# Performance work log

Measured on AMD Instinct MI355X. Metric: run time of the kernel, lower is better.

The kernel has to match this reference:

```python
import jax, jax.numpy as jnp
import numpy as np

NTYPES = 8
EXCLUDE = [(0, 1), (2, 3)]
NF, NLOC, NNEI = 4, 16384, 128
NALL = 32768


def _build_type_mask(ntypes, exclude):
    ex = set()
    for a, b in exclude:
        ex.add((a, b))
        ex.add((b, a))
    tm = np.ones((ntypes + 1, ntypes + 1), dtype=np.float32)
    for ti, tj in ex:
        tm[tj, ti] = 0.0
    return tm.reshape(-1)  # flattened [(ntypes+1)^2]


def setup_inputs() -> dict:
    key = jax.random.key(0)
    k1, k2 = jax.random.split(key)
    # nlist in [-1, NALL): -1 marks a missing neighbor
    nlist = jax.random.randint(k1, (NF, NLOC, NNEI), -1, NALL, dtype=jnp.int32)
    atype_ext = jax.random.randint(k2, (NF, NALL), 0, NTYPES, dtype=jnp.int32)
    type_mask = jnp.asarray(_build_type_mask(NTYPES, EXCLUDE))
    return {"nlist": nlist, "atype_ext": atype_ext, "type_mask": type_mask, "ntypes": NTYPES}


def reference(nlist, atype_ext, type_mask, ntypes):
    nf, nloc, nnei = nlist.shape
    nall = atype_ext.shape[1]
    # append virtual type `ntypes` used for -1 (padding) neighbors
    ae = jnp.concatenate(
        [atype_ext, jnp.full((nf, 1), ntypes, dtype=atype_ext.dtype)], axis=-1
    )  # [nf, nall+1]
    type_i = atype_ext[:, :nloc] * (ntypes + 1)  # [nf, nloc]
    index = jnp.where(nlist == -1, nall, nlist)  # [nf, nloc, nnei]
    type_j = jnp.take_along_axis(ae, index.reshape(nf, nloc * nnei), axis=1)
    type_j = type_j.reshape(nf, nloc, nnei)
    type_ij = type_i[:, :, None] + type_j  # flat index into type_mask table
    mask = type_mask[type_ij]  # [nf, nloc, nnei]
    return mask
```

## Files before the change

kernel.cpp:

```cpp
#include <hip/hip_runtime.h>

#define NF    4
#define NLOC  16384
#define NNEI  128
#define NALL  32768
#define TMASK_LDS 96

#define ELEMS_PER_FRAME (NLOC * NNEI)
#define Q4_PER_FRAME    (ELEMS_PER_FRAME / 4)
#define BLOCKS_PER_FRAME 256
#define THREADS 256
#define ITERS (Q4_PER_FRAME / (BLOCKS_PER_FRAME * THREADS))

__global__ void __launch_bounds__(256) build_type_table(
    const int* __restrict__ atype_ext,
    unsigned char* __restrict__ ttab)
{
    const int t = blockIdx.x * blockDim.x + threadIdx.x;
    const int4 v = reinterpret_cast<const int4*>(atype_ext)[t];
    uchar4 b;
    b.x = (unsigned char)v.x;
    b.y = (unsigned char)v.y;
    b.z = (unsigned char)v.z;
    b.w = (unsigned char)v.w;
    reinterpret_cast<uchar4*>(ttab)[t] = b;
}

__global__ void __launch_bounds__(THREADS) pair_exclude_mask_kernel(
    const int* __restrict__ nlist,
    const unsigned char* __restrict__ ttab,
    const float* __restrict__ type_mask,
    const int* __restrict__ ntypes_p,
    float* __restrict__ out)
{
    __shared__ unsigned char stt[NALL];
    __shared__ float smask[TMASK_LDS];

    const int f = blockIdx.x / BLOCKS_PER_FRAME;
    const int b = blockIdx.x % BLOCKS_PER_FRAME;

    {
        const uint4* src = reinterpret_cast<const uint4*>(ttab + (size_t)f * NALL);
        uint4* dst = reinterpret_cast<uint4*>(stt);
        #pragma unroll
        for (int k = 0; k < NALL / 16 / THREADS; ++k)
            dst[threadIdx.x + k * THREADS] = src[threadIdx.x + k * THREADS];
        if (threadIdx.x < 81) smask[threadIdx.x] = type_mask[threadIdx.x];
    }
    __syncthreads();

    const int ntypes = ntypes_p[0];
    const int np1 = ntypes + 1;

    const int* nl_base = nlist + (size_t)f * ELEMS_PER_FRAME;
    float* out_base = out + (size_t)f * ELEMS_PER_FRAME;
    const int q0 = b * (THREADS * ITERS);

    #pragma unroll
    for (int it = 0; it < ITERS; ++it) {
        const int q = q0 + it * THREADS + threadIdx.x;
        const int4 nl = reinterpret_cast<const int4*>(nl_base)[q];
        const int e = q * 4;
        const int i = e >> 7;
        const int ti = (int)stt[i] * np1;

        float4 m;
        {
            const int tj = (nl.x == -1) ? ntypes : (int)stt[nl.x];
            m.x = smask[ti + tj];
        }
        {
            const int tj = (nl.y == -1) ? ntypes : (int)stt[nl.y];
            m.y = smask[ti + tj];
        }
        {
            const int tj = (nl.z == -1) ? ntypes : (int)stt[nl.z];
            m.z = smask[ti + tj];
        }
        {
            const int tj = (nl.w == -1) ? ntypes : (int)stt[nl.w];
            m.w = smask[ti + tj];
        }
        reinterpret_cast<float4*>(out_base)[q] = m;
    }
}

extern "C" void kernel_launch(void* const* d_in, const int* in_sizes, int n_in,
                              void* d_out, int out_size, void* d_ws, size_t ws_size,
                              hipStream_t stream) {
    const int*   nlist     = (const int*)d_in[0];
    const int*   atype_ext = (const int*)d_in[1];
    const float* type_mask = (const float*)d_in[2];
    const int*   ntypes_p  = (const int*)d_in[3];
    float*       out       = (float*)d_out;
    unsigned char* ttab    = (unsigned char*)d_ws;

    build_type_table<<<(NF * NALL / 4) / 256, 256, 0, stream>>>(atype_ext, ttab);

    pair_exclude_mask_kernel<<<NF * BLOCKS_PER_FRAME, THREADS, 0, stream>>>(
        nlist, ttab, type_mask, ntypes_p, out);
}
```

Measured before the change: 91.21 us.

## Precompute per-atom column bitmasks so mask lookup becomes a bit test

The preprocessing kernel now stores, for each extended atom, a byte bitmask over center types showing which pairs are allowed, plus a padding entry for the virtual -1 neighbor type. The main kernel replaces the two-level table lookup (type load, then mask table load) with one LDS byte load and a shift. It uses 512 threads with all four int4 loads issued up front, and reads the center type straight from atype_ext. The bitmask caps ntypes at 8, and the -1 handling relies on an unsigned min clamp to index NALL.

```diff
diff --git a/kernel.cpp b/kernel.cpp
--- a/kernel.cpp
+++ b/kernel.cpp
@@ -4,37 +4,52 @@
 #define NLOC  16384
 #define NNEI  128
 #define NALL  32768
-#define TMASK_LDS 96
 
 #define ELEMS_PER_FRAME (NLOC * NNEI)
 #define Q4_PER_FRAME    (ELEMS_PER_FRAME / 4)
+#define THREADS 512
 #define BLOCKS_PER_FRAME 256
-#define THREADS 256
 #define ITERS (Q4_PER_FRAME / (BLOCKS_PER_FRAME * THREADS))
 
-__global__ void __launch_bounds__(256) build_type_table(
+__global__ void __launch_bounds__(256) build_colbits(
     const int* __restrict__ atype_ext,
+    const float* __restrict__ type_mask,
+    const int* __restrict__ ntypes_p,
     unsigned char* __restrict__ ttab)
 {
     const int t = blockIdx.x * blockDim.x + threadIdx.x;
+    const int ntypes = ntypes_p[0];
+    const int np1 = ntypes + 1;
+
     const int4 v = reinterpret_cast<const int4*>(atype_ext)[t];
+    unsigned bx = 0, by = 0, bz = 0, bw = 0;
+    for (int i = 0; i < ntypes; ++i) {
+        const float* row = type_mask + i * np1;
+        bx |= (row[v.x] != 0.0f ? 1u : 0u) << i;
+        by |= (row[v.y] != 0.0f ? 1u : 0u) << i;
+        bz |= (row[v.z] != 0.0f ? 1u : 0u) << i;
+        bw |= (row[v.w] != 0.0f ? 1u : 0u) << i;
+    }
     uchar4 b;
-    b.x = (unsigned char)v.x;
-    b.y = (unsigned char)v.y;
-    b.z = (unsigned char)v.z;
-    b.w = (unsigned char)v.w;
+    b.x = (unsigned char)bx; b.y = (unsigned char)by;
+    b.z = (unsigned char)bz; b.w = (unsigned char)bw;
     reinterpret_cast<uchar4*>(ttab)[t] = b;
+
+    if (t == 0) {
+        unsigned bp = 0;
+        for (int i = 0; i < ntypes; ++i)
+            bp |= (type_mask[i * np1 + ntypes] != 0.0f ? 1u : 0u) << i;
+        ttab[(size_t)NF * NALL] = (unsigned char)bp;
+    }
 }
 
 __global__ void __launch_bounds__(THREADS) pair_exclude_mask_kernel(
     const int* __restrict__ nlist,
     const unsigned char* __restrict__ ttab,
-    const float* __restrict__ type_mask,
-    const int* __restrict__ ntypes_p,
+    const int* __restrict__ atype_ext,
     float* __restrict__ out)
 {
-    __shared__ unsigned char stt[NALL];
-    __shared__ float smask[TMASK_LDS];
+    __shared__ unsigned char stt[NALL + 4];
 
     const int f = blockIdx.x / BLOCKS_PER_FRAME;
     const int b = blockIdx.x % BLOCKS_PER_FRAME;
@@ -45,44 +60,48 @@
         #pragma unroll
         for (int k = 0; k < NALL / 16 / THREADS; ++k)
             dst[threadIdx.x + k * THREADS] = src[threadIdx.x + k * THREADS];
-        if (threadIdx.x < 81) smask[threadIdx.x] = type_mask[threadIdx.x];
+        if (threadIdx.x == 0) stt[NALL] = ttab[(size_t)NF * NALL];
     }
     __syncthreads();
 
-    const int ntypes = ntypes_p[0];
-    const int np1 = ntypes + 1;
-
     const int* nl_base = nlist + (size_t)f * ELEMS_PER_FRAME;
     float* out_base = out + (size_t)f * ELEMS_PER_FRAME;
+    const int* at_base = atype_ext + (size_t)f * NALL;
     const int q0 = b * (THREADS * ITERS);
 
-    #pragma unroll
-    for (int it = 0; it < ITERS; ++it) {
-        const int q = q0 + it * THREADS + threadIdx.x;
-        const int4 nl = reinterpret_cast<const int4*>(nl_base)[q];
-        const int e = q * 4;
-        const int i = e >> 7;
-        const int ti = (int)stt[i] * np1;
+    const int qA = q0 + 0 * THREADS + threadIdx.x;
+    const int qB = q0 + 1 * THREADS + threadIdx.x;
+    const int qC = q0 + 2 * THREADS + threadIdx.x;
+    const int qD = q0 + 3 * THREADS + threadIdx.x;
 
-        float4 m;
-        {
-            const int tj = (nl.x == -1) ? ntypes : (int)stt[nl.x];
-            m.x = smask[ti + tj];
-        }
-        {
-            const int tj = (nl.y == -1) ? ntypes : (int)stt[nl.y];
-            m.y = smask[ti + tj];
-        }
-        {
-            const int tj = (nl.z == -1) ? ntypes : (int)stt[nl.z];
-            m.z = smask[ti + tj];
-        }
-        {
-            const int tj = (nl.w == -1) ? ntypes : (int)stt[nl.w];
-            m.w = smask[ti + tj];
-        }
-        reinterpret_cast<float4*>(out_base)[q] = m;
+    const int4 nlA = reinterpret_cast<const int4*>(nl_base)[qA];
+    const int4 nlB = reinterpret_cast<const int4*>(nl_base)[qB];
+    const int4 nlC = reinterpret_cast<const int4*>(nl_base)[qC];
+    const int4 nlD = reinterpret_cast<const int4*>(nl_base)[qD];
+    const int tiA = at_base[qA >> 5];
+    const int tiB = at_base[qB >> 5];
+    const int tiC = at_base[qC >> 5];
+    const int tiD = at_base[qD >> 5];
+
+#define DO4(nl, ti, q)                                                        \
+    {                                                                         \
+        const unsigned ix = min((unsigned)nl.x, (unsigned)NALL);              \
+        const unsigned iy = min((unsigned)nl.y, (unsigned)NALL);              \
+        const unsigned iz = min((unsigned)nl.z, (unsigned)NALL);              \
+        const unsigned iw = min((unsigned)nl.w, (unsigned)NALL);              \
+        float4 m;                                                             \
+        m.x = (float)((stt[ix] >> ti) & 1);                                   \
+        m.y = (float)((stt[iy] >> ti) & 1);                                   \
+        m.z = (float)((stt[iz] >> ti) & 1);                                   \
+        m.w = (float)((stt[iw] >> ti) & 1);                                   \
+        reinterpret_cast<float4*>(out_base)[q] = m;                           \
     }
+
+    DO4(nlA, tiA, qA)
+    DO4(nlB, tiB, qB)
+    DO4(nlC, tiC, qC)
+    DO4(nlD, tiD, qD)
+#undef DO4
 }
 
 extern "C" void kernel_launch(void* const* d_in, const int* in_sizes, int n_in,
@@ -95,8 +114,9 @@
     float*       out       = (float*)d_out;
     unsigned char* ttab    = (unsigned char*)d_ws;
 
-    build_type_table<<<(NF * NALL / 4) / 256, 256, 0, stream>>>(atype_ext, ttab);
+    build_colbits<<<(NF * NALL / 4) / 256, 256, 0, stream>>>(
+        atype_ext, type_mask, ntypes_p, ttab);
 
     pair_exclude_mask_kernel<<<NF * BLOCKS_PER_FRAME, THREADS, 0, stream>>>(
-        nlist, ttab, type_mask, ntypes_p, out);
+        nlist, ttab, atype_ext, out);
 }
```

New measurement: 91.91 us, median of 2. About the same (+0.8%).
